# Optimization experiments

Measured on AMD Instinct MI355X. Metric: run time of the kernel, lower is better.

## Reference

```python
import jax, jax.numpy as jnp
import numpy as np

N_HEADS = 16
N_EMB = 1024
HEAD_SIZE = 64
BLOCK_SIZE = 2048


def setup_inputs() -> dict:
    key = jax.random.key(0)
    k1, k2, k3, k4, k5 = jax.random.split(key, 5)
    B, T, E, H, D = 4, BLOCK_SIZE, N_EMB, N_HEADS, HEAD_SIZE
    s = 1.0 / np.sqrt(E)
    x = jax.random.normal(k1, (B, T, E), dtype=jnp.float32)
    # Stacked per-head projection weights (Linear with bias=False): [H, E, D]
    Wq = jax.random.normal(k2, (H, E, D), dtype=jnp.float32) * s
    Wk = jax.random.normal(k3, (H, E, D), dtype=jnp.float32) * s
    Wv = jax.random.normal(k4, (H, E, D), dtype=jnp.float32) * s
    Wo = jax.random.normal(k5, (H * D, E), dtype=jnp.float32) * (1.0 / np.sqrt(H * D))
    return {"x": x, "Wq": Wq, "Wk": Wk, "Wv": Wv, "Wo": Wo}


def reference(x, Wq, Wk, Wv, Wo):
    # x: [B,T,E]; Wq/Wk/Wv: [H,E,D]; Wo: [H*D,E]
    B, T, E = x.shape
    H, _, D = Wq.shape
    q = jnp.einsum('bte,hed->bhtd', x, Wq)
    k = jnp.einsum('bte,hed->bhtd', x, Wk)
    v = jnp.einsum('bte,hed->bhtd', x, Wv)
    scores = jnp.einsum('bhtd,bhsd->bhts', q, k) * (D ** -0.5)  # [B,H,T,T]
    causal = jnp.tril(jnp.ones((T, T), dtype=bool))
    scores = jnp.where(causal, scores, -jnp.inf)
    wei = jax.nn.softmax(scores, axis=-1)  # dropout is identity in eval mode
    out = jnp.einsum('bhts,bhsd->bhtd', wei, v)  # [B,H,T,D]
    out = out.transpose(0, 2, 1, 3).reshape(B, T, H * D)  # concat heads
    return out @ Wo  # [B,T,E]
```

## Files before the change

### kernel.cpp

```cpp
#include <hip/hip_runtime.h>

#define B_  4
#define T_  2048
#define E_  1024
#define H_  16
#define D_  64
#define HD_ 1024
#define BT_ 8192

typedef __bf16 bf16x8 __attribute__((ext_vector_type(8)));
typedef float  f32x4  __attribute__((ext_vector_type(4)));

static __device__ __forceinline__ unsigned short f2bf(float f) {
  __bf16 h = (__bf16)f;
  return __builtin_bit_cast(unsigned short, h);
}
static __device__ __forceinline__ bf16x8 ldb8(const unsigned short* p) {
  return *(const bf16x8*)p;
}

#define GLD_LDS16(gp, lp)                                                      \
  __builtin_amdgcn_global_load_lds(                                            \
      (const __attribute__((address_space(1))) void*)(gp),                     \
      (__attribute__((address_space(3))) void*)(lp), 16, 0, 0)


__global__ __launch_bounds__(256) void cast_x_k(const float* __restrict__ x,
                                                unsigned short* __restrict__ xb) {
  int i = blockIdx.x * 256 + threadIdx.x;
  float4 v = ((const float4*)x)[i];
  ushort4 o;
  o.x = f2bf(v.x); o.y = f2bf(v.y); o.z = f2bf(v.z); o.w = f2bf(v.w);
  ((ushort4*)xb)[i] = o;
}

__global__ __launch_bounds__(256) void cast_wqkv_k(const float* __restrict__ Wq,
                                                   const float* __restrict__ Wk,
                                                   const float* __restrict__ Wv,
                                                   unsigned short* __restrict__ wT) {
  int tid = blockIdx.x * 256 + threadIdx.x;
  int e = tid & (E_ - 1);
  int d = (tid >> 10) & (D_ - 1);
  int h = (tid >> 16) & (H_ - 1);
  int w = tid >> 20;
  const float* src = (w == 0) ? Wq : (w == 1) ? Wk : Wv;
  wT[tid] = f2bf(src[(h * E_ + e) * D_ + d]);
}

__global__ __launch_bounds__(256) void cast_wo_k(const float* __restrict__ Wo,
                                                 unsigned short* __restrict__ woT) {
  int tid = blockIdx.x * 256 + threadIdx.x;
  int hd = tid & (HD_ - 1);
  int e  = tid >> 10;
  woT[tid] = f2bf(Wo[hd * E_ + e]);
}

static __device__ __forceinline__ void gemm_core(const unsigned short* __restrict__ A,
                                                 const unsigned short* __restrict__ BT,
                                                 const int K, const int m0, const int n0,
                                                 unsigned short* lA, unsigned short* lB,
                                                 f32x4 acc[4][4]) {
  const int tid  = threadIdx.x;
  const int wave = tid >> 6;
  const int lane = tid & 63;
  const int wm = wave & 1, wn = wave >> 1;
  const int l16 = lane & 15, quad = lane >> 4;

  const unsigned short* gA = A + (size_t)(m0 + (tid >> 2)) * K + (tid & 3) * 8;
  const unsigned short* gB = BT + (size_t)(n0 + (tid >> 2)) * K + (tid & 3) * 8;

  #pragma unroll
  for (int i = 0; i < 4; ++i)
    #pragma unroll
    for (int j = 0; j < 4; ++j) acc[i][j] = (f32x4){0.f, 0.f, 0.f, 0.f};

  const int nit = K >> 5;
  GLD_LDS16(gA, lA + wave * 512);
  GLD_LDS16(gA + (size_t)64 * K, lA + 2048 + wave * 512);
  GLD_LDS16(gB, lB + wave * 512);
  GLD_LDS16(gB + (size_t)64 * K, lB + 2048 + wave * 512);

  for (int it = 0; it < nit; ++it) {
    __syncthreads();
    if (it + 1 < nit) {
      const int kb = (it + 1) * 32;
      const int nb = ((it + 1) & 1) * 4096;
      GLD_LDS16(gA + kb, lA + nb + wave * 512);
      GLD_LDS16(gA + (size_t)64 * K + kb, lA + nb + 2048 + wave * 512);
      GLD_LDS16(gB + kb, lB + nb + wave * 512);
      GLD_LDS16(gB + (size_t)64 * K + kb, lB + nb + 2048 + wave * 512);
    }
    const unsigned short* cA = lA + (it & 1) * 4096;
    const unsigned short* cB = lB + (it & 1) * 4096;
    bf16x8 aF[4], bF[4];
    #pragma unroll
    for (int i = 0; i < 4; ++i)
      aF[i] = ldb8(cA + (wm * 64 + i * 16 + l16) * 32 + quad * 8);
    #pragma unroll
    for (int j = 0; j < 4; ++j)
      bF[j] = ldb8(cB + (wn * 64 + j * 16 + l16) * 32 + quad * 8);
    #pragma unroll
    for (int i = 0; i < 4; ++i)
      #pragma unroll
      for (int j = 0; j < 4; ++j)
        acc[i][j] = __builtin_amdgcn_mfma_f32_16x16x32_bf16(aF[i], bF[j], acc[i][j], 0, 0, 0);
  }
}

__global__ __launch_bounds__(256) void qkv_gemm_k(const unsigned short* __restrict__ xb,
                                                  const unsigned short* __restrict__ wT,
                                                  unsigned short* __restrict__ q,
                                                  unsigned short* __restrict__ k,
                                                  unsigned short* __restrict__ vT) {
  __shared__ unsigned short lA[2 * 128 * 32], lB[2 * 128 * 32];
  f32x4 acc[4][4];
  const int m0 = blockIdx.x * 128, n0 = blockIdx.y * 128;
  gemm_core(xb, wT, E_, m0, n0, lA, lB, acc);

  const int wave = threadIdx.x >> 6, lane = threadIdx.x & 63;
  const int wm = wave & 1, wn = wave >> 1;
  const int l16 = lane & 15, quad = lane >> 4;
  const int type = n0 >> 10;
  const float C = 0.18033688011112042f;
  #pragma unroll
  for (int i = 0; i < 4; ++i) {
    #pragma unroll
    for (int j = 0; j < 4; ++j) {
      const int n = n0 + wn * 64 + j * 16 + l16;
      const int h = (n >> 6) & 15, d = n & 63;
      #pragma unroll
      for (int r = 0; r < 4; ++r) {
        const int m = m0 + wm * 64 + i * 16 + quad * 4 + r;
        const int b = m >> 11, t = m & (T_ - 1);
        if (type == 0)
          q[((size_t)(b * H_ + h) * T_ + t) * D_ + d] = f2bf(acc[i][j][r] * C);
        else if (type == 1)
          k[((size_t)(b * H_ + h) * T_ + t) * D_ + d] = f2bf(acc[i][j][r]);
        else
          vT[((size_t)(b * H_ + h) * D_ + d) * T_ + t] = f2bf(acc[i][j][r]);
      }
    }
  }
}

__global__ __launch_bounds__(256) void proj_k(const unsigned short* __restrict__ ao,
                                              const unsigned short* __restrict__ woT,
                                              float* __restrict__ out) {
  __shared__ unsigned short lA[2 * 128 * 32], lB[2 * 128 * 32];
  f32x4 acc[4][4];
  const int m0 = blockIdx.x * 128, n0 = blockIdx.y * 128;
  gemm_core(ao, woT, HD_, m0, n0, lA, lB, acc);

  const int wave = threadIdx.x >> 6, lane = threadIdx.x & 63;
  const int wm = wave & 1, wn = wave >> 1;
  const int l16 = lane & 15, quad = lane >> 4;
  #pragma unroll
  for (int i = 0; i < 4; ++i)
    #pragma unroll
    for (int j = 0; j < 4; ++j)
      #pragma unroll
      for (int r = 0; r < 4; ++r)
        out[(size_t)(m0 + wm * 64 + i * 16 + quad * 4 + r) * E_ +
            n0 + wn * 64 + j * 16 + l16] = acc[i][j][r];
}

__global__ __launch_bounds__(256) void attn_k(const unsigned short* __restrict__ q,
                                              const unsigned short* __restrict__ k,
                                              const unsigned short* __restrict__ vT,
                                              unsigned short* __restrict__ ao) {
  __shared__ unsigned short lK[2][64 * 64];
  __shared__ unsigned short lV[2][64 * 64];
  __shared__ unsigned short lP[4][32][72];
  const int tid  = threadIdx.x;
  const int lane = tid & 63;
  const int wave = tid >> 6;
  const int l16  = lane & 15;
  const int quad = lane >> 4;
  const int id    = (int)blockIdx.x;
  const int bhid  = id & 63;
  const int qpair = id >> 6;
  const int h = bhid & 15, b = bhid >> 4;
  const size_t bh = (size_t)(b * H_ + h);
  const unsigned short* qp = q  + bh * (T_ * D_);
  const unsigned short* kp = k  + bh * (T_ * D_);
  const unsigned short* vp = vT + bh * (D_ * T_);

  const int srow = tid >> 3;
  const int kseg = (tid & 7) ^ (srow & 7);
  const int sw = (l16 & 7);

  #pragma unroll
  for (int pr = 0; pr < 2; ++pr) {
    const int qblk = (pr == 0) ? qpair : 15 - qpair;
    const int q0 = qblk * 128 + wave * 32;

    bf16x8 aq[2][2];
    #pragma unroll
    for (int rb = 0; rb < 2; ++rb)
      #pragma unroll
      for (int hh = 0; hh < 2; ++hh)
        aq[rb][hh] = ldb8(qp + (q0 + rb * 16 + l16) * D_ + hh * 32 + quad * 8);

    float lr[2][4];
    f32x4 o[2][4];
    #pragma unroll
    for (int rb = 0; rb < 2; ++rb) {
      #pragma unroll
      for (int r = 0; r < 4; ++r) lr[rb][r] = 0.f;
      #pragma unroll
      for (int nb = 0; nb < 4; ++nb) o[rb][nb] = (f32x4){0.f, 0.f, 0.f, 0.f};
    }

    const int nch = 2 * (qblk + 1);

    {
      unsigned short* Kb = lK[0];
      unsigned short* Vb = lV[0];
      GLD_LDS16(kp + srow * D_ + kseg * 8, Kb + wave * 512);
      GLD_LDS16(kp + (32 + srow) * D_ + kseg * 8, Kb + 2048 + wave * 512);
      GLD_LDS16(vp + (size_t)srow * T_ + kseg * 8, Vb + wave * 512);
      GLD_LDS16(vp + (size_t)(32 + srow) * T_ + kseg * 8, Vb + 2048 + wave * 512);
    }

    for (int c = 0; c < nch; ++c) {
      __syncthreads();
      if (c + 1 < nch) {
        const int s1 = (c + 1) * 64;
        unsigned short* Kb = lK[(c + 1) & 1];
        unsigned short* Vb = lV[(c + 1) & 1];
        GLD_LDS16(kp + (s1 + srow) * D_ + kseg * 8, Kb + wave * 512);
        GLD_LDS16(kp + (s1 + 32 + srow) * D_ + kseg * 8, Kb + 2048 + wave * 512);
        GLD_LDS16(vp + (size_t)srow * T_ + s1 + kseg * 8, Vb + wave * 512);
        GLD_LDS16(vp + (size_t)(32 + srow) * T_ + s1 + kseg * 8, Vb + 2048 + wave * 512);
      }
      const int s0 = c * 64;
      const unsigned short* Kb = lK[c & 1];
      const unsigned short* Vb = lV[c & 1];
      f32x4 sc[2][4];
      #pragma unroll
      for (int rb = 0; rb < 2; ++rb)
        #pragma unroll
        for (int j = 0; j < 4; ++j) sc[rb][j] = (f32x4){0.f, 0.f, 0.f, 0.f};
      #pragma unroll
      for (int j = 0; j < 4; ++j) {
        const int sr = j * 16 + l16;
        bf16x8 bk0 = ldb8(Kb + sr * 64 + ((quad ^ sw) << 3));
        bf16x8 bk1 = ldb8(Kb + sr * 64 + (((4 + quad) ^ sw) << 3));
        #pragma unroll
        for (int rb = 0; rb < 2; ++rb) {
          sc[rb][j] = __builtin_amdgcn_mfma_f32_16x16x32_bf16(aq[rb][0], bk0, sc[rb][j], 0, 0, 0);
          sc[rb][j] = __builtin_amdgcn_mfma_f32_16x16x32_bf16(aq[rb][1], bk1, sc[rb][j], 0, 0, 0);
        }
      }
      const bool domask = (c == nch - 1) || (c == nch - 2);
      #pragma unroll
      for (int rb = 0; rb < 2; ++rb) {
        #pragma unroll
        for (int j = 0; j < 4; ++j) {
          #pragma unroll
          for (int r = 0; r < 4; ++r) {
            float p = __builtin_amdgcn_exp2f(sc[rb][j][r]);
            if (domask) {
              const int qg = q0 + rb * 16 + quad * 4 + r;
              if (s0 + j * 16 + l16 > qg) p = 0.f;
            }
            lr[rb][r] += p;
            lP[wave][rb * 16 + quad * 4 + r][j * 16 + l16] = f2bf(p);
          }
        }
      }
      __builtin_amdgcn_wave_barrier();
      bf16x8 aP[2][2];
      #pragma unroll
      for (int rb = 0; rb < 2; ++rb)
        #pragma unroll
        for (int hh = 0; hh < 2; ++hh)
          aP[rb][hh] = ldb8(&lP[wave][rb * 16 + l16][hh * 32 + quad * 8]);
      __builtin_amdgcn_wave_barrier();
      #pragma unroll
      for (int nb = 0; nb < 4; ++nb) {
        const int d = nb * 16 + l16;
        bf16x8 bV0 = ldb8(Vb + d * 64 + ((quad ^ sw) << 3));
        bf16x8 bV1 = ldb8(Vb + d * 64 + (((4 + quad) ^ sw) << 3));
        #pragma unroll
        for (int rb = 0; rb < 2; ++rb) {
          o[rb][nb] = __builtin_amdgcn_mfma_f32_16x16x32_bf16(aP[rb][0], bV0, o[rb][nb], 0, 0, 0);
          o[rb][nb] = __builtin_amdgcn_mfma_f32_16x16x32_bf16(aP[rb][1], bV1, o[rb][nb], 0, 0, 0);
        }
      }
    }

    #pragma unroll
    for (int off = 1; off < 16; off <<= 1)
      #pragma unroll
      for (int rb = 0; rb < 2; ++rb)
        #pragma unroll
        for (int r = 0; r < 4; ++r)
          lr[rb][r] += __shfl_xor(lr[rb][r], off, 64);
    #pragma unroll
    for (int rb = 0; rb < 2; ++rb) {
      #pragma unroll
      for (int r = 0; r < 4; ++r) {
        const float inv = 1.0f / lr[rb][r];
        const int t = q0 + rb * 16 + quad * 4 + r;
        #pragma unroll
        for (int nb = 0; nb < 4; ++nb)
          ao[((size_t)(b * T_ + t) * H_ + h) * D_ + nb * 16 + l16] = f2bf(o[rb][nb][r] * inv);
      }
    }
  }
}


extern "C" void kernel_launch(void* const* d_in, const int* in_sizes, int n_in,
                              void* d_out, int out_size, void* d_ws, size_t ws_size,
                              hipStream_t stream) {
  const float* x  = (const float*)d_in[0];
  const float* Wq = (const float*)d_in[1];
  const float* Wk = (const float*)d_in[2];
  const float* Wv = (const float*)d_in[3];
  const float* Wo = (const float*)d_in[4];
  float* out = (float*)d_out;

  char* ws = (char*)d_ws;
  unsigned short* xb   = (unsigned short*)(ws + 0);
  unsigned short* wT   = (unsigned short*)(ws + 16777216);
  unsigned short* woT  = (unsigned short*)(ws + 23068672);
  unsigned short* qb   = (unsigned short*)(ws + 25165824);
  unsigned short* kb   = (unsigned short*)(ws + 41943040);
  unsigned short* vTb  = (unsigned short*)(ws + 58720256);
  unsigned short* aob  = (unsigned short*)(ws + 75497472);

  cast_x_k<<<dim3((BT_ * E_) / 4 / 256), dim3(256), 0, stream>>>(x, xb);
  cast_wqkv_k<<<dim3((3 * H_ * D_ * E_) / 256), dim3(256), 0, stream>>>(Wq, Wk, Wv, wT);
  cast_wo_k<<<dim3((E_ * HD_) / 256), dim3(256), 0, stream>>>(Wo, woT);
  qkv_gemm_k<<<dim3(BT_ / 128, 3072 / 128), dim3(256), 0, stream>>>(xb, wT, qb, kb, vTb);
  attn_k<<<dim3(512), dim3(256), 0, stream>>>(qb, kb, vTb, aob);
  proj_k<<<dim3(BT_ / 128, E_ / 128), dim3(256), 0, stream>>>(aob, woT, out);
}
```

Before: 283.1 us.

## Merge cast kernels with LDS-tiled transposes and widen GEMM K-tile with swizzle

Three cast and transpose kernels become one prep kernel, which transposes the weights through a padded shared-memory tile so both reads and writes are coalesced. The shared GEMM core moves from a 32-wide to a 64-wide K step, using an XOR-swizzled LDS layout to avoid bank conflicts and raising MFMA priority around the compute block. The aim is fewer launches, fewer strided global accesses, and half as many barriers per GEMM. In exchange, LDS use doubles to 64KB per GEMM block, which may reduce occupancy.

Measured after the change: 252.8 us. 10.7% less time.

```diff
diff --git a/kernel.cpp b/kernel.cpp
--- a/kernel.cpp
+++ b/kernel.cpp
@@ -24,35 +24,84 @@
       (const __attribute__((address_space(1))) void*)(gp),                     \
       (__attribute__((address_space(3))) void*)(lp), 16, 0, 0)
 
-
-__global__ __launch_bounds__(256) void cast_x_k(const float* __restrict__ x,
-                                                unsigned short* __restrict__ xb) {
-  int i = blockIdx.x * 256 + threadIdx.x;
-  float4 v = ((const float4*)x)[i];
-  ushort4 o;
-  o.x = f2bf(v.x); o.y = f2bf(v.y); o.z = f2bf(v.z); o.w = f2bf(v.w);
-  ((ushort4*)xb)[i] = o;
-}
-
-__global__ __launch_bounds__(256) void cast_wqkv_k(const float* __restrict__ Wq,
-                                                   const float* __restrict__ Wk,
-                                                   const float* __restrict__ Wv,
-                                                   unsigned short* __restrict__ wT) {
-  int tid = blockIdx.x * 256 + threadIdx.x;
-  int e = tid & (E_ - 1);
-  int d = (tid >> 10) & (D_ - 1);
-  int h = (tid >> 16) & (H_ - 1);
-  int w = tid >> 20;
-  const float* src = (w == 0) ? Wq : (w == 1) ? Wk : Wv;
-  wT[tid] = f2bf(src[(h * E_ + e) * D_ + d]);
-}
-
-__global__ __launch_bounds__(256) void cast_wo_k(const float* __restrict__ Wo,
-                                                 unsigned short* __restrict__ woT) {
-  int tid = blockIdx.x * 256 + threadIdx.x;
-  int hd = tid & (HD_ - 1);
-  int e  = tid >> 10;
-  woT[tid] = f2bf(Wo[hd * E_ + e]);
+__global__ __launch_bounds__(256) void prep_k(const float* __restrict__ x,
+                                              const float* __restrict__ Wq,
+                                              const float* __restrict__ Wk,
+                                              const float* __restrict__ Wv,
+                                              const float* __restrict__ Wo,
+                                              unsigned short* __restrict__ xb,
+                                              unsigned short* __restrict__ wT,
+                                              unsigned short* __restrict__ woT) {
+  const int bid = blockIdx.x, tid = threadIdx.x;
+  if (bid < 2048) {
+    #pragma unroll
+    for (int p = 0; p < 4; ++p) {
+      int i = bid * 1024 + p * 256 + tid;
+      float4 v = ((const float4*)x)[i];
+      ushort4 o;
+      o.x = f2bf(v.x); o.y = f2bf(v.y); o.z = f2bf(v.z); o.w = f2bf(v.w);
+      ((ushort4*)xb)[i] = o;
+    }
+    return;
+  }
+  __shared__ float tl[64 * 65];
+  if (bid < 2816) {
+    const int tix = bid - 2048;
+    const int w = tix >> 8;
+    const int h = (tix >> 4) & 15;
+    const int e0 = (tix & 15) * 64;
+    const float* src = (w == 0) ? Wq : (w == 1) ? Wk : Wv;
+    #pragma unroll
+    for (int rr = 0; rr < 4; ++rr) {
+      const int e = e0 + rr * 16 + (tid >> 4);
+      const int d4 = (tid & 15) * 4;
+      float4 v = *(const float4*)&src[(size_t)(h * 1024 + e) * 64 + d4];
+      tl[(e - e0) * 65 + d4 + 0] = v.x;
+      tl[(e - e0) * 65 + d4 + 1] = v.y;
+      tl[(e - e0) * 65 + d4 + 2] = v.z;
+      tl[(e - e0) * 65 + d4 + 3] = v.w;
+    }
+    __syncthreads();
+    #pragma unroll
+    for (int cc = 0; cc < 4; ++cc) {
+      const int d = cc * 16 + (tid >> 4);
+      const int e4 = (tid & 15) * 4;
+      ushort4 o;
+      o.x = f2bf(tl[(e4 + 0) * 65 + d]);
+      o.y = f2bf(tl[(e4 + 1) * 65 + d]);
+      o.z = f2bf(tl[(e4 + 2) * 65 + d]);
+      o.w = f2bf(tl[(e4 + 3) * 65 + d]);
+      *(ushort4*)&wT[(size_t)((w * 16 + h) * 64 + d) * 1024 + e0 + e4] = o;
+    }
+    return;
+  }
+  {
+    const int tix = bid - 2816;
+    const int hd0 = (tix >> 4) * 64;
+    const int e0 = (tix & 15) * 64;
+    #pragma unroll
+    for (int rr = 0; rr < 4; ++rr) {
+      const int hd = hd0 + rr * 16 + (tid >> 4);
+      const int e4 = (tid & 15) * 4;
+      float4 v = *(const float4*)&Wo[(size_t)hd * 1024 + e0 + e4];
+      tl[(hd - hd0) * 65 + e4 + 0] = v.x;
+      tl[(hd - hd0) * 65 + e4 + 1] = v.y;
+      tl[(hd - hd0) * 65 + e4 + 2] = v.z;
+      tl[(hd - hd0) * 65 + e4 + 3] = v.w;
+    }
+    __syncthreads();
+    #pragma unroll
+    for (int cc = 0; cc < 4; ++cc) {
+      const int e = e0 + cc * 16 + (tid >> 4);
+      const int hd4 = (tid & 15) * 4;
+      ushort4 o;
+      o.x = f2bf(tl[(hd4 + 0) * 65 + (e - e0)]);
+      o.y = f2bf(tl[(hd4 + 1) * 65 + (e - e0)]);
+      o.z = f2bf(tl[(hd4 + 2) * 65 + (e - e0)]);
+      o.w = f2bf(tl[(hd4 + 3) * 65 + (e - e0)]);
+      *(ushort4*)&woT[(size_t)e * 1024 + hd0 + hd4] = o;
+    }
+  }
 }
 
 static __device__ __forceinline__ void gemm_core(const unsigned short* __restrict__ A,
@@ -65,46 +114,65 @@
   const int lane = tid & 63;
   const int wm = wave & 1, wn = wave >> 1;
   const int l16 = lane & 15, quad = lane >> 4;
-
-  const unsigned short* gA = A + (size_t)(m0 + (tid >> 2)) * K + (tid & 3) * 8;
-  const unsigned short* gB = BT + (size_t)(n0 + (tid >> 2)) * K + (tid & 3) * 8;
+  const int nkt = K >> 6;
+
+  const int sr = tid >> 3;
+  const int sc = ((tid & 7) ^ (sr & 7)) * 8;
+  const int sw = l16 & 7;
+  const int sl0 = (quad ^ sw) << 3;
+  const int sl1 = ((4 + quad) ^ sw) << 3;
+
+#define STG(kt) do {                                                            \
+    const size_t kb = (size_t)(kt) * 64 + sc;                                   \
+    unsigned short* dA = lA + ((kt) & 1) * 8192 + wave * 512;                   \
+    unsigned short* dB = lB + ((kt) & 1) * 8192 + wave * 512;                   \
+    GLD_LDS16(A  + (size_t)(m0 +      sr) * K + kb, dA);                        \
+    GLD_LDS16(A  + (size_t)(m0 + 32 + sr) * K + kb, dA + 2048);                 \
+    GLD_LDS16(A  + (size_t)(m0 + 64 + sr) * K + kb, dA + 4096);                 \
+    GLD_LDS16(A  + (size_t)(m0 + 96 + sr) * K + kb, dA + 6144);                 \
+    GLD_LDS16(BT + (size_t)(n0 +      sr) * K + kb, dB);                        \
+    GLD_LDS16(BT + (size_t)(n0 + 32 + sr) * K + kb, dB + 2048);                 \
+    GLD_LDS16(BT + (size_t)(n0 + 64 + sr) * K + kb, dB + 4096);                 \
+    GLD_LDS16(BT + (size_t)(n0 + 96 + sr) * K + kb, dB + 6144);                 \
+  } while (0)
 
   #pragma unroll
   for (int i = 0; i < 4; ++i)
     #pragma unroll
     for (int j = 0; j < 4; ++j) acc[i][j] = (f32x4){0.f, 0.f, 0.f, 0.f};
 
-  const int nit = K >> 5;
-  GLD_LDS16(gA, lA + wave * 512);
-  GLD_LDS16(gA + (size_t)64 * K, lA + 2048 + wave * 512);
-  GLD_LDS16(gB, lB + wave * 512);
-  GLD_LDS16(gB + (size_t)64 * K, lB + 2048 + wave * 512);
-
-  for (int it = 0; it < nit; ++it) {
+  STG(0);
+  for (int kt = 0; kt < nkt; ++kt) {
     __syncthreads();
-    if (it + 1 < nit) {
-      const int kb = (it + 1) * 32;
-      const int nb = ((it + 1) & 1) * 4096;
-      GLD_LDS16(gA + kb, lA + nb + wave * 512);
-      GLD_LDS16(gA + (size_t)64 * K + kb, lA + nb + 2048 + wave * 512);
-      GLD_LDS16(gB + kb, lB + nb + wave * 512);
-      GLD_LDS16(gB + (size_t)64 * K + kb, lB + nb + 2048 + wave * 512);
-    }
-    const unsigned short* cA = lA + (it & 1) * 4096;
-    const unsigned short* cB = lB + (it & 1) * 4096;
-    bf16x8 aF[4], bF[4];
-    #pragma unroll
-    for (int i = 0; i < 4; ++i)
-      aF[i] = ldb8(cA + (wm * 64 + i * 16 + l16) * 32 + quad * 8);
-    #pragma unroll
-    for (int j = 0; j < 4; ++j)
-      bF[j] = ldb8(cB + (wn * 64 + j * 16 + l16) * 32 + quad * 8);
-    #pragma unroll
-    for (int i = 0; i < 4; ++i)
-      #pragma unroll
-      for (int j = 0; j < 4; ++j)
-        acc[i][j] = __builtin_amdgcn_mfma_f32_16x16x32_bf16(aF[i], bF[j], acc[i][j], 0, 0, 0);
-  }
+    if (kt + 1 < nkt) STG(kt + 1);
+    const unsigned short* cA = lA + (kt & 1) * 8192;
+    const unsigned short* cB = lB + (kt & 1) * 8192;
+    bf16x8 aF[4][2], bF[4][2];
+    #pragma unroll
+    for (int mi = 0; mi < 4; ++mi) {
+      const int ar = (wm * 64 + mi * 16 + l16) * 64;
+      aF[mi][0] = ldb8(cA + ar + sl0);
+      aF[mi][1] = ldb8(cA + ar + sl1);
+    }
+    #pragma unroll
+    for (int nj = 0; nj < 4; ++nj) {
+      const int br = (wn * 64 + nj * 16 + l16) * 64;
+      bF[nj][0] = ldb8(cB + br + sl0);
+      bF[nj][1] = ldb8(cB + br + sl1);
+    }
+    __builtin_amdgcn_s_setprio(1);
+    #pragma unroll
+    for (int mi = 0; mi < 4; ++mi)
+      #pragma unroll
+      for (int nj = 0; nj < 4; ++nj) {
+        acc[mi][nj] = __builtin_amdgcn_mfma_f32_16x16x32_bf16(aF[mi][0], bF[nj][0],
+                                                              acc[mi][nj], 0, 0, 0);
+        acc[mi][nj] = __builtin_amdgcn_mfma_f32_16x16x32_bf16(aF[mi][1], bF[nj][1],
+                                                              acc[mi][nj], 0, 0, 0);
+      }
+    __builtin_amdgcn_s_setprio(0);
+  }
+#undef STG
 }
 
 __global__ __launch_bounds__(256) void qkv_gemm_k(const unsigned short* __restrict__ xb,
@@ -112,7 +180,7 @@
                                                   unsigned short* __restrict__ q,
                                                   unsigned short* __restrict__ k,
                                                   unsigned short* __restrict__ vT) {
-  __shared__ unsigned short lA[2 * 128 * 32], lB[2 * 128 * 32];
+  __shared__ unsigned short lA[2 * 128 * 64], lB[2 * 128 * 64];
   f32x4 acc[4][4];
   const int m0 = blockIdx.x * 128, n0 = blockIdx.y * 128;
   gemm_core(xb, wT, E_, m0, n0, lA, lB, acc);
@@ -146,7 +214,7 @@
 __global__ __launch_bounds__(256) void proj_k(const unsigned short* __restrict__ ao,
                                               const unsigned short* __restrict__ woT,
                                               float* __restrict__ out) {
-  __shared__ unsigned short lA[2 * 128 * 32], lB[2 * 128 * 32];
+  __shared__ unsigned short lA[2 * 128 * 64], lB[2 * 128 * 64];
   f32x4 acc[4][4];
   const int m0 = blockIdx.x * 128, n0 = blockIdx.y * 128;
   gemm_core(ao, woT, HD_, m0, n0, lA, lB, acc);
@@ -331,9 +399,7 @@
   unsigned short* vTb  = (unsigned short*)(ws + 58720256);
   unsigned short* aob  = (unsigned short*)(ws + 75497472);
 
-  cast_x_k<<<dim3((BT_ * E_) / 4 / 256), dim3(256), 0, stream>>>(x, xb);
-  cast_wqkv_k<<<dim3((3 * H_ * D_ * E_) / 256), dim3(256), 0, stream>>>(Wq, Wk, Wv, wT);
-  cast_wo_k<<<dim3((E_ * HD_) / 256), dim3(256), 0, stream>>>(Wo, woT);
+  prep_k<<<dim3(3072), dim3(256), 0, stream>>>(x, Wq, Wk, Wv, Wo, xb, wT, woT);
   qkv_gemm_k<<<dim3(BT_ / 128, 3072 / 128), dim3(256), 0, stream>>>(xb, wT, qb, kb, vTb);
   attn_k<<<dim3(512), dim3(256), 0, stream>>>(qb, kb, vTb, aob);
   proj_k<<<dim3(BT_ / 128, E_ / 128), dim3(256), 0, stream>>>(aob, woT, out);
```
